# Optimization experiments

Hardware: AMD Instinct MI355X
Metric: run time of the kernel (lower is better)

The kernel has to match this reference:

```python
import jax, jax.numpy as jnp
import numpy as np

T_TOTAL = 90  # t_total init arg (static decode length)


def _gru_cell(x, h, w_ih, w_hh, b_ih, b_hh):
    # PyTorch nn.GRUCell math
    gi = x @ w_ih.T + b_ih
    gh = h @ w_hh.T + b_hh
    i_r, i_z, i_n = jnp.split(gi, 3, axis=-1)
    h_r, h_z, h_n = jnp.split(gh, 3, axis=-1)
    r = jax.nn.sigmoid(i_r + h_r)
    z = jax.nn.sigmoid(i_z + h_z)
    n = jnp.tanh(i_n + r * h_n)
    return (1.0 - z) * n + z * h


def setup_inputs() -> dict:
    key = jax.random.key(0)
    T, B, NX, H, NZ = 90, 2048, 144, 128, 128
    M1, M2 = 300, 200
    ks = jax.random.split(key, 24)
    def p(k, shape):
        return jax.random.normal(k, shape, dtype=jnp.float32) * 0.05
    return {
        "x": jax.random.normal(ks[0], (T, B, NX), dtype=jnp.float32),
        # encoder GRUCell (nx -> H)
        "w_ih_e": p(ks[1], (3 * H, NX)), "w_hh_e": p(ks[2], (3 * H, H)),
        "b_ih_e": p(ks[3], (3 * H,)),   "b_hh_e": p(ks[4], (3 * H,)),
        # encoder MLP (tanh) H->300->200
        "W1e": p(ks[5], (M1, H)),  "b1e": p(ks[6], (M1,)),
        "W2e": p(ks[7], (M2, M1)), "b2e": p(ks[8], (M2,)),
        # latent heads 200->NZ
        "Wmu": p(ks[9], (NZ, M2)),  "bmu": p(ks[10], (NZ,)),
        "Wlv": p(ks[11], (NZ, M2)), "blv": p(ks[12], (NZ,)),
        # decoder GRUCell (nx+nz -> H)
        "w_ih_d": p(ks[13], (3 * H, NX + NZ)), "w_hh_d": p(ks[14], (3 * H, H)),
        "b_ih_d": p(ks[15], (3 * H,)),          "b_hh_d": p(ks[16], (3 * H,)),
        # decoder MLP (tanh) H->300->200 and output 200->nx
        "W1d": p(ks[17], (M1, H)),  "b1d": p(ks[18], (M1,)),
        "W2d": p(ks[19], (M2, M1)), "b2d": p(ks[20], (M2,)),
        "Wo": p(ks[21], (NX, M2)),  "bo": p(ks[22], (NX,)),
    }


def reference(x, w_ih_e, w_hh_e, b_ih_e, b_hh_e, W1e, b1e, W2e, b2e,
              Wmu, bmu, Wlv, blv, w_ih_d, w_hh_d, b_ih_d, b_hh_d,
              W1d, b1d, W2d, b2d, Wo, bo):
    B = x.shape[1]
    H = w_hh_e.shape[1]
    h0 = jnp.zeros((B, H), dtype=x.dtype)

    # ---- encode: GRU over time, take last hidden ----
    def enc_step(h, xt):
        return _gru_cell(xt, h, w_ih_e, w_hh_e, b_ih_e, b_hh_e), None
    h_x, _ = jax.lax.scan(enc_step, h0, x)  # (B, H)
    he = jnp.tanh(h_x @ W1e.T + b1e)
    he = jnp.tanh(he @ W2e.T + b2e)
    mu = he @ Wmu.T + bmu
    logvar = he @ Wlv.T + blv
    z = mu  # eval mode: z = mu (no reparameterization noise)

    def dec_step(carry, _):
        hd, xp = carry
        rnn_in = jnp.concatenate([xp, z], axis=1)  # (B, NX+NZ)
        hd = _gru_cell(rnn_in, hd, w_ih_d, w_hh_d, b_ih_d, b_hh_d)
        m = jnp.tanh(hd @ W1d.T + b1d)
        m = jnp.tanh(m @ W2d.T + b2d)
        xi = m @ Wo.T + bo
        return (hd, xi), xi

    _, x_rec = jax.lax.scan(dec_step, (h0, x[0]), None, length=T_TOTAL)
    return x_rec, mu, logvar
```

## Files before the change

### kernel.cpp

```cpp
#include <hip/hip_runtime.h>
#include <cstddef>

#define T_STEPS 90
#define BT      2048
#define NXV     144
#define HV      128
#define NZV     128
#define M1V     300
#define M2V     200
#define NB      16
#define NTH     512

typedef __attribute__((ext_vector_type(8))) _Float16 half8v;
typedef __attribute__((ext_vector_type(4))) float f32x4;

constexpr int MTa[12]   = {24,24,19,13, 8, 8,24,24,24,19,13, 9};
constexpr int MREAL[12] = {384,384,300,200,128,128,384,384,384,300,200,144};
constexpr int KREAL[12] = {144,128,128,300,200,200,144,128,128,128,300,200};
constexpr int RSW[12]   = {144,128,128,300,200,200,272,272,128,128,300,200};
constexpr int COW[12]   = {  0,  0,  0,  0,  0,  0,  0,144,  0,  0,  0,  0};
constexpr int P13[13]   = {0,120,240,335,465,521,577,697,817,937,1032,1162,1225};
constexpr int NFRAG = 1225;

__device__ __forceinline__ float fsig(float v)  { return 1.0f / (1.0f + __expf(-v)); }
__device__ __forceinline__ float ftanh(float v) { return 1.0f - 2.0f / (__expf(2.0f * v) + 1.0f); }

__global__ void __launch_bounds__(64)
prep_frags(const float* __restrict__ w_ih_e, const float* __restrict__ w_hh_e,
           const float* __restrict__ W1e,    const float* __restrict__ W2e,
           const float* __restrict__ Wmu,    const float* __restrict__ Wlv,
           const float* __restrict__ w_ih_d, const float* __restrict__ w_hh_d,
           const float* __restrict__ W1d,    const float* __restrict__ W2d,
           const float* __restrict__ Wo,
           const float* __restrict__ b_ih_e, const float* __restrict__ b_hh_e,
           const float* __restrict__ b1e,    const float* __restrict__ b2e,
           const float* __restrict__ bmu,    const float* __restrict__ blv,
           const float* __restrict__ b_ih_d, const float* __restrict__ b_hh_d,
           const float* __restrict__ b1d,    const float* __restrict__ b2d,
           const float* __restrict__ bo,
           _Float16* __restrict__ ws)
{
    int f = blockIdx.x;
    int g = 0;
    while (g < 11 && f >= P13[g + 1]) ++g;
    int fl = f - P13[g];
    int MT = MTa[g];
    int kt = fl / MT, mt = fl - kt * MT;

    const float* W; const float* bias;
    switch (g) {
        case 0:  W = w_ih_e; bias = b_ih_e; break;
        case 1:  W = w_hh_e; bias = b_hh_e; break;
        case 2:  W = W1e;    bias = b1e;    break;
        case 3:  W = W2e;    bias = b2e;    break;
        case 4:  W = Wmu;    bias = bmu;    break;
        case 5:  W = Wlv;    bias = blv;    break;
        case 6:  W = w_ih_d; bias = nullptr; break;
        case 7:  W = w_ih_d; bias = b_ih_d; break;
        case 8:  W = w_hh_d; bias = b_hh_d; break;
        case 9:  W = W1d;    bias = b1d;    break;
        case 10: W = W2d;    bias = b2d;    break;
        default: W = Wo;     bias = bo;     break;
    }
    int l = threadIdx.x;
    int m  = mt * 16 + (l & 15);
    int kb = kt * 32 + (l >> 4) * 8;
    _Float16* dst = ws + (size_t)f * 512 + (size_t)l * 8;
    #pragma unroll
    for (int j = 0; j < 8; ++j) {
        int k = kb + j;
        float val = 0.0f;
        if (m < MREAL[g]) {
            if (k < KREAL[g]) val = W[(size_t)m * RSW[g] + COW[g] + k];
            else if (k == KREAL[g] && bias) val = bias[m];
        }
        dst[j] = (_Float16)val;
    }
}

template<int RS>
__device__ __forceinline__ void gate_gemm_reg(const half8v (&gw)[15],
                                              const _Float16* __restrict__ Bt,
                                              int l, f32x4 (&acc)[3])
{
    const int bo_ = (l & 15) * RS + ((l >> 4) << 3);
    #pragma unroll
    for (int kt = 0; kt < 5; ++kt) {
        half8v bf = *(const half8v*)(Bt + bo_ + kt * 32);
        #pragma unroll
        for (int j = 0; j < 3; ++j)
            acc[j] = __builtin_amdgcn_mfma_f32_16x16x32_f16(gw[kt * 3 + j], bf, acc[j], 0, 0, 0);
    }
}

template<int MT, int KT, int NT, int RS>
__device__ __forceinline__ void mlp_stream(const half8v* __restrict__ A,
                                           const _Float16* __restrict__ Bt,
                                           int w, int l, f32x4 (&acc)[NT])
{
    half8v af[NT * KT];
    #pragma unroll
    for (int i = 0; i < NT; ++i) {
        int mt = w + 8 * i;
        if (mt < MT) {
            #pragma unroll
            for (int kt = 0; kt < KT; ++kt)
                af[i * KT + kt] = A[(size_t)(kt * MT + mt) * 64 + l];
        }
    }
    const int bo_ = (l & 15) * RS + ((l >> 4) << 3);
    #pragma unroll
    for (int kt = 0; kt < KT; ++kt) {
        half8v bf = *(const half8v*)(Bt + bo_ + kt * 32);
        #pragma unroll
        for (int i = 0; i < NT; ++i) {
            int mt = w + 8 * i;
            if (mt < MT)
                acc[i] = __builtin_amdgcn_mfma_f32_16x16x32_f16(af[i * KT + kt], bf, acc[i], 0, 0, 0);
        }
    }
}

template<int MT, int KT, int NT, int RS>
__device__ __forceinline__ void mlp_lds(const _Float16* __restrict__ Alds,
                                        const _Float16* __restrict__ Bt,
                                        int w, int l, f32x4 (&acc)[NT])
{
    const int bo_ = (l & 15) * RS + ((l >> 4) << 3);
    #pragma unroll
    for (int kt = 0; kt < KT; ++kt) {
        half8v bf = *(const half8v*)(Bt + bo_ + kt * 32);
        #pragma unroll
        for (int i = 0; i < NT; ++i) {
            int mt = w + 8 * i;
            if (mt < MT) {
                half8v af = *(const half8v*)(Alds + ((size_t)(kt * MT + mt) * 64 + l) * 8);
                acc[i] = __builtin_amdgcn_mfma_f32_16x16x32_f16(af, bf, acc[i], 0, 0, 0);
            }
        }
    }
}

template<int MT, int NT, int RS>
__device__ __forceinline__ void write_tanhN(const f32x4 (&acc)[NT], int Mreal,
                                            _Float16* __restrict__ T, int w, int l)
{
    int b = l & 15, q4 = (l >> 4) << 2;
    #pragma unroll
    for (int i = 0; i < NT; ++i) {
        int mt = w + 8 * i;
        if (mt < MT) {
            #pragma unroll
            for (int r = 0; r < 4; ++r) {
                int m = mt * 16 + q4 + r;
                if (m < Mreal) T[b * RS + m] = (_Float16)ftanh(acc[i][r]);
            }
        }
    }
}

__global__ void __launch_bounds__(NTH, 2)
vae_mfma(const float* __restrict__ x, const half8v* __restrict__ wsv,
         float* __restrict__ out)
{
    __shared__ __align__(16) _Float16 xT [NB * 168];
    __shared__ __align__(16) _Float16 hT [NB * 168];
    __shared__ __align__(16) _Float16 m1T[NB * 328];
    __shared__ __align__(16) _Float16 m2T[NB * 232];
    __shared__ __align__(16) _Float16 g10L[130 * 512];

    const int tid = threadIdx.x;
    const int w = tid >> 6, l = tid & 63;
    const int bbase = blockIdx.x * NB;
    const size_t XREC_SZ = (size_t)T_STEPS * BT * NXV;
    const size_t MU_OFF = XREC_SZ;
    const size_t LV_OFF = XREC_SZ + (size_t)BT * NZV;
    const f32x4 z4 = {0.f, 0.f, 0.f, 0.f};

#define AHI(g) (wsv + (size_t)P13[g] * 64)

    auto load_x = [&](int t, float xr[5]) {
        #pragma unroll
        for (int u = 0; u < 5; ++u) {
            int i = u * NTH + tid;
            if (i < NB * NXV)
                xr[u] = __builtin_nontemporal_load(
                    &x[(size_t)t * (BT * NXV) + (size_t)(bbase + i / NXV) * NXV + (i % NXV)]);
        }
    };
    auto store_x = [&](const float xr[5]) {
        #pragma unroll
        for (int u = 0; u < 5; ++u) {
            int i = u * NTH + tid;
            if (i < NB * NXV) {
                int b2 = i / NXV, k = i - b2 * NXV;
                xT[b2 * 168 + k] = (_Float16)xr[u];
            }
        }
    };

    half8v gih[15], ghh[15];
    auto load_gates = [&](const half8v* Gih, const half8v* Ghh) {
        #pragma unroll
        for (int kt = 0; kt < 5; ++kt) {
            #pragma unroll
            for (int j = 0; j < 3; ++j) {
                gih[kt * 3 + j] = Gih[(size_t)(kt * 24 + w + 8 * j) * 64 + l];
                ghh[kt * 3 + j] = Ghh[(size_t)(kt * 24 + w + 8 * j) * 64 + l];
            }
        }
    };

    float hreg[4] = {0.f, 0.f, 0.f, 0.f};
    auto gru_combine = [&](const f32x4 (&ai)[3], const f32x4 (&ah)[3]) {
        #pragma unroll
        for (int r = 0; r < 4; ++r) {
            float rr = fsig(ai[0][r] + ah[0][r]);
            float zz = fsig(ai[1][r] + ah[1][r]);
            float nn = ftanh(ai[2][r] + rr * ah[2][r]);
            hreg[r] = (1.f - zz) * nn + zz * hreg[r];
        }
    };
    auto write_h = [&]() {
        int jb = 16 * w + ((l >> 4) << 2), b = l & 15;
        #pragma unroll
        for (int r = 0; r < 4; ++r) hT[b * 168 + jb + r] = (_Float16)hreg[r];
    };

    for (int i = tid; i < NB * 168; i += NTH) { xT[i] = (_Float16)0.f; hT[i] = (_Float16)0.f; }
    for (int i = tid; i < NB * 328; i += NTH) m1T[i] = (_Float16)0.f;
    for (int i = tid; i < NB * 232; i += NTH) m2T[i] = (_Float16)0.f;
    for (int i = tid; i < 130 * 64; i += NTH)
        *(half8v*)(g10L + (size_t)i * 8) = AHI(10)[i];
    load_gates(AHI(0), AHI(1));
    float xrA[5] = {0, 0, 0, 0, 0}, xrB[5] = {0, 0, 0, 0, 0};
    load_x(0, xrA);
    __syncthreads();
    if (tid < NB) {
        xT [tid * 168 + 144] = (_Float16)1.f;
        hT [tid * 168 + 128] = (_Float16)1.f;
        m1T[tid * 328 + 300] = (_Float16)1.f;
        m2T[tid * 232 + 200] = (_Float16)1.f;
    }
    store_x(xrA);
    load_x(1, xrA);
    __syncthreads();

    for (int t = 0; t < T_STEPS; t += 2) {
        {
            if (t + 2 < T_STEPS) load_x(t + 2, xrB);
            f32x4 ai[3] = {z4, z4, z4}, ah[3] = {z4, z4, z4};
            gate_gemm_reg<168>(gih, xT, l, ai);
            gate_gemm_reg<168>(ghh, hT, l, ah);
            gru_combine(ai, ah);
            __syncthreads();
            write_h();
            if (t + 1 < T_STEPS) store_x(xrA);
            __syncthreads();
        }
        {
            if (t + 3 < T_STEPS) load_x(t + 3, xrA);
            f32x4 ai[3] = {z4, z4, z4}, ah[3] = {z4, z4, z4};
            gate_gemm_reg<168>(gih, xT, l, ai);
            gate_gemm_reg<168>(ghh, hT, l, ah);
            gru_combine(ai, ah);
            __syncthreads();
            write_h();
            if (t + 2 < T_STEPS) store_x(xrB);
            __syncthreads();
        }
    }

    {
        f32x4 a1[3] = {z4, z4, z4};
        mlp_stream<19, 5, 3, 168>(AHI(2), hT, w, l, a1);
        write_tanhN<19, 3, 328>(a1, M1V, m1T, w, l);
        __syncthreads();
        f32x4 a2[2] = {z4, z4};
        mlp_stream<13, 10, 2, 328>(AHI(3), m1T, w, l, a2);
        write_tanhN<13, 2, 232>(a2, M2V, m2T, w, l);
        __syncthreads();
        f32x4 am[1] = {z4}, av[1] = {z4};
        mlp_stream<8, 7, 1, 232>(AHI(4), m2T, w, l, am);
        mlp_stream<8, 7, 1, 232>(AHI(5), m2T, w, l, av);
        __syncthreads();
        int b = l & 15, q4 = (l >> 4) << 2;
        int m = w * 16 + q4;
        __builtin_nontemporal_store(am[0], (f32x4*)&out[MU_OFF + (size_t)(bbase + b) * NZV + m]);
        __builtin_nontemporal_store(av[0], (f32x4*)&out[LV_OFF + (size_t)(bbase + b) * NZV + m]);
        #pragma unroll
        for (int r = 0; r < 4; ++r)
            m1T[b * 328 + m + r] = (_Float16)am[0][r];
    }

    f32x4 gzr[3] = {z4, z4, z4};
    {
        for (int i = tid; i < NB * HV; i += NTH) {
            int b2 = i >> 7, j = i & 127;
            hT[b2 * 168 + j] = (_Float16)0.f;
        }
        if (tid < NB) m1T[tid * 328 + 128] = (_Float16)1.f;
        float xr0[5] = {0, 0, 0, 0, 0};
        load_x(0, xr0);
        store_x(xr0);
        __syncthreads();
        mlp_stream<24, 5, 3, 328>(AHI(7), m1T, w, l, gzr);
        load_gates(AHI(6), AHI(8));
        #pragma unroll
        for (int r = 0; r < 4; ++r) hreg[r] = 0.f;
    }
    __syncthreads();

    f32x4 aop[2] = {z4, z4};
    for (int t = 0; t < T_STEPS; ++t) {
        if (t > 0 && w < 9) {
            int b = l & 15, q4 = (l >> 4) << 2;
            #pragma unroll
            for (int i2 = 0; i2 < 2; ++i2) {
                int mt = w + 8 * i2;
                if (mt < 9)
                    __builtin_nontemporal_store(aop[i2],
                        (f32x4*)&out[(size_t)(t - 1) * (BT * NXV) + (size_t)(bbase + b) * NXV + mt * 16 + q4]);
            }
        }
        f32x4 ai[3], ah[3];
        #pragma unroll
        for (int i = 0; i < 3; ++i) { ai[i] = gzr[i]; ah[i] = z4; }
        gate_gemm_reg<168>(gih, xT, l, ai);
        gate_gemm_reg<168>(ghh, hT, l, ah);
        gru_combine(ai, ah);
        __syncthreads();
        write_h();
        __syncthreads();
        f32x4 a1[3] = {z4, z4, z4};
        mlp_stream<19, 5, 3, 168>(AHI(9), hT, w, l, a1);
        write_tanhN<19, 3, 328>(a1, M1V, m1T, w, l);
        __syncthreads();
        f32x4 a2[2] = {z4, z4};
        mlp_lds<13, 10, 2, 328>(g10L, m1T, w, l, a2);
        write_tanhN<13, 2, 232>(a2, M2V, m2T, w, l);
        __syncthreads();
        f32x4 ao[2] = {z4, z4};
        mlp_stream<9, 7, 2, 232>(AHI(11), m2T, w, l, ao);
        {
            int b = l & 15, q4 = (l >> 4) << 2;
            #pragma unroll
            for (int i2 = 0; i2 < 2; ++i2) {
                int mt = w + 8 * i2;
                if (mt < 9) {
                    int m = mt * 16 + q4;
                    #pragma unroll
                    for (int r = 0; r < 4; ++r)
                        xT[b * 168 + m + r] = (_Float16)ao[i2][r];
                    aop[i2] = ao[i2];
                }
            }
        }
        __syncthreads();
    }
    if (w < 9) {
        int b = l & 15, q4 = (l >> 4) << 2;
        #pragma unroll
        for (int i2 = 0; i2 < 2; ++i2) {
            int mt = w + 8 * i2;
            if (mt < 9)
                __builtin_nontemporal_store(aop[i2],
                    (f32x4*)&out[(size_t)(T_STEPS - 1) * (BT * NXV) + (size_t)(bbase + b) * NXV + mt * 16 + q4]);
        }
    }
#undef AHI
}

extern "C" void kernel_launch(void* const* d_in, const int* in_sizes, int n_in,
                              void* d_out, int out_size, void* d_ws, size_t ws_size,
                              hipStream_t stream) {
    (void)in_sizes; (void)n_in; (void)out_size; (void)ws_size;
    const float* p[23];
    for (int i = 0; i < 23; ++i) p[i] = (const float*)d_in[i];
    _Float16* ws = (_Float16*)d_ws;

    prep_frags<<<dim3(NFRAG), dim3(64), 0, stream>>>(
        p[1], p[2], p[5], p[7], p[9], p[11], p[13], p[14], p[17], p[19], p[21],
        p[3], p[4], p[6], p[8], p[10], p[12], p[15], p[16], p[18], p[20], p[22],
        ws);

    vae_mfma<<<dim3(BT / NB), dim3(NTH), 0, stream>>>(
        p[0], (const half8v*)ws, (float*)d_out);
}
```

Baseline: 866.2 us.

## Double-buffer decoder hidden state and prefetch output-layer weights into registers

Makes the decoder hidden-state LDS tile double-buffered (ping-pong on step parity), which removes one block barrier per decode step before writing h. It also shrinks the LDS copy of the W2d weights by one K-tile, streaming that last tile from global into registers early, and prefetches all Wo fragments into registers before the W2d GEMM so the output GEMM runs from registers. These changes hide global-load latency and drop a sync, in exchange for extra LDS for the second h buffer and higher register pressure that could lower occupancy at launch bounds (512, 2).

```diff
diff --git a/kernel.cpp b/kernel.cpp
--- a/kernel.cpp
+++ b/kernel.cpp
@@ -164,10 +164,10 @@
          float* __restrict__ out)
 {
     __shared__ __align__(16) _Float16 xT [NB * 168];
-    __shared__ __align__(16) _Float16 hT [NB * 168];
+    __shared__ __align__(16) _Float16 hT [2][NB * 168];
     __shared__ __align__(16) _Float16 m1T[NB * 328];
     __shared__ __align__(16) _Float16 m2T[NB * 232];
-    __shared__ __align__(16) _Float16 g10L[130 * 512];
+    __shared__ __align__(16) _Float16 g10L[117 * 512];
 
     const int tid = threadIdx.x;
     const int w = tid >> 6, l = tid & 63;
@@ -221,16 +221,16 @@
             hreg[r] = (1.f - zz) * nn + zz * hreg[r];
         }
     };
-    auto write_h = [&]() {
+    auto write_h = [&](int p) {
         int jb = 16 * w + ((l >> 4) << 2), b = l & 15;
         #pragma unroll
-        for (int r = 0; r < 4; ++r) hT[b * 168 + jb + r] = (_Float16)hreg[r];
+        for (int r = 0; r < 4; ++r) hT[p][b * 168 + jb + r] = (_Float16)hreg[r];
     };
 
-    for (int i = tid; i < NB * 168; i += NTH) { xT[i] = (_Float16)0.f; hT[i] = (_Float16)0.f; }
+    for (int i = tid; i < NB * 168; i += NTH) { xT[i] = (_Float16)0.f; hT[0][i] = (_Float16)0.f; hT[1][i] = (_Float16)0.f; }
     for (int i = tid; i < NB * 328; i += NTH) m1T[i] = (_Float16)0.f;
     for (int i = tid; i < NB * 232; i += NTH) m2T[i] = (_Float16)0.f;
-    for (int i = tid; i < 130 * 64; i += NTH)
+    for (int i = tid; i < 117 * 64; i += NTH)
         *(half8v*)(g10L + (size_t)i * 8) = AHI(10)[i];
     load_gates(AHI(0), AHI(1));
     float xrA[5] = {0, 0, 0, 0, 0}, xrB[5] = {0, 0, 0, 0, 0};
@@ -238,7 +238,8 @@
     __syncthreads();
     if (tid < NB) {
         xT [tid * 168 + 144] = (_Float16)1.f;
-        hT [tid * 168 + 128] = (_Float16)1.f;
+        hT[0][tid * 168 + 128] = (_Float16)1.f;
+        hT[1][tid * 168 + 128] = (_Float16)1.f;
         m1T[tid * 328 + 300] = (_Float16)1.f;
         m2T[tid * 232 + 200] = (_Float16)1.f;
     }
@@ -251,10 +252,10 @@
             if (t + 2 < T_STEPS) load_x(t + 2, xrB);
             f32x4 ai[3] = {z4, z4, z4}, ah[3] = {z4, z4, z4};
             gate_gemm_reg<168>(gih, xT, l, ai);
-            gate_gemm_reg<168>(ghh, hT, l, ah);
+            gate_gemm_reg<168>(ghh, hT[0], l, ah);
             gru_combine(ai, ah);
             __syncthreads();
-            write_h();
+            write_h(0);
             if (t + 1 < T_STEPS) store_x(xrA);
             __syncthreads();
         }
@@ -262,10 +263,10 @@
             if (t + 3 < T_STEPS) load_x(t + 3, xrA);
             f32x4 ai[3] = {z4, z4, z4}, ah[3] = {z4, z4, z4};
             gate_gemm_reg<168>(gih, xT, l, ai);
-            gate_gemm_reg<168>(ghh, hT, l, ah);
+            gate_gemm_reg<168>(ghh, hT[0], l, ah);
             gru_combine(ai, ah);
             __syncthreads();
-            write_h();
+            write_h(0);
             if (t + 2 < T_STEPS) store_x(xrB);
             __syncthreads();
         }
@@ -273,7 +274,7 @@
 
     {
         f32x4 a1[3] = {z4, z4, z4};
-        mlp_stream<19, 5, 3, 168>(AHI(2), hT, w, l, a1);
+        mlp_stream<19, 5, 3, 168>(AHI(2), hT[0], w, l, a1);
         write_tanhN<19, 3, 328>(a1, M1V, m1T, w, l);
         __syncthreads();
         f32x4 a2[2] = {z4, z4};
@@ -297,7 +298,7 @@
     {
         for (int i = tid; i < NB * HV; i += NTH) {
             int b2 = i >> 7, j = i & 127;
-            hT[b2 * 168 + j] = (_Float16)0.f;
+            hT[0][b2 * 168 + j] = (_Float16)0.f;
         }
         if (tid < NB) m1T[tid * 328 + 128] = (_Float16)1.f;
         float xr0[5] = {0, 0, 0, 0, 0};
@@ -313,6 +314,7 @@
 
     f32x4 aop[2] = {z4, z4};
     for (int t = 0; t < T_STEPS; ++t) {
+        const int q = t & 1;
         if (t > 0 && w < 9) {
             int b = l & 15, q4 = (l >> 4) << 2;
             #pragma unroll
@@ -327,21 +329,51 @@
         #pragma unroll
         for (int i = 0; i < 3; ++i) { ai[i] = gzr[i]; ah[i] = z4; }
         gate_gemm_reg<168>(gih, xT, l, ai);
-        gate_gemm_reg<168>(ghh, hT, l, ah);
+        gate_gemm_reg<168>(ghh, hT[q], l, ah);
         gru_combine(ai, ah);
-        __syncthreads();
-        write_h();
-        __syncthreads();
+        write_h(q ^ 1);
+        __syncthreads();
+        half8v w2f9[2];
+        #pragma unroll
+        for (int i = 0; i < 2; ++i)
+            if (w + 8 * i < 13)
+                w2f9[i] = AHI(10)[(size_t)(9 * 13 + w + 8 * i) * 64 + l];
         f32x4 a1[3] = {z4, z4, z4};
-        mlp_stream<19, 5, 3, 168>(AHI(9), hT, w, l, a1);
+        mlp_stream<19, 5, 3, 168>(AHI(9), hT[q ^ 1], w, l, a1);
         write_tanhN<19, 3, 328>(a1, M1V, m1T, w, l);
         __syncthreads();
+        half8v wo_af[14];
+        #pragma unroll
+        for (int kt = 0; kt < 7; ++kt) {
+            #pragma unroll
+            for (int i = 0; i < 2; ++i)
+                if (w + 8 * i < 9)
+                    wo_af[kt * 2 + i] = AHI(11)[(size_t)(kt * 9 + w + 8 * i) * 64 + l];
+        }
         f32x4 a2[2] = {z4, z4};
-        mlp_lds<13, 10, 2, 328>(g10L, m1T, w, l, a2);
+        mlp_lds<13, 9, 2, 328>(g10L, m1T, w, l, a2);
+        {
+            const int bo2 = (l & 15) * 328 + ((l >> 4) << 3);
+            half8v bf = *(const half8v*)(m1T + bo2 + 9 * 32);
+            #pragma unroll
+            for (int i = 0; i < 2; ++i)
+                if (w + 8 * i < 13)
+                    a2[i] = __builtin_amdgcn_mfma_f32_16x16x32_f16(w2f9[i], bf, a2[i], 0, 0, 0);
+        }
         write_tanhN<13, 2, 232>(a2, M2V, m2T, w, l);
         __syncthreads();
         f32x4 ao[2] = {z4, z4};
-        mlp_stream<9, 7, 2, 232>(AHI(11), m2T, w, l, ao);
+        {
+            const int bo_ = (l & 15) * 232 + ((l >> 4) << 3);
+            #pragma unroll
+            for (int kt = 0; kt < 7; ++kt) {
+                half8v bf = *(const half8v*)(m2T + bo_ + kt * 32);
+                #pragma unroll
+                for (int i = 0; i < 2; ++i)
+                    if (w + 8 * i < 9)
+                        ao[i] = __builtin_amdgcn_mfma_f32_16x16x32_f16(wo_af[kt * 2 + i], bf, ao[i], 0, 0, 0);
+            }
+        }
         {
             int b = l & 15, q4 = (l >> 4) << 2;
             #pragma unroll
```

New measurement: 1.091 ms. 26.0% more time.

## Fold decoder output projection into next-step GRU input weights

Applied to the files above, without the earlier changes.

Precomputes combined weights (w_ih_d[:, :NX] @ Wo, plus the bias term) in the prep kernel so that each decoder step's input gate consumes the MLP hidden m2 directly instead of the reconstructed output. This removes the per-step write of the output into the xT LDS buffer and one block barrier, and decouples the output GEMM from the next step's gate computation. In exchange, the input gate GEMM now streams K=200 weights from memory rather than using register-resident K=144 fragments, and fp16 rounding differs.

```diff
diff --git a/kernel.cpp b/kernel.cpp
--- a/kernel.cpp
+++ b/kernel.cpp
@@ -21,6 +21,7 @@
 constexpr int COW[12]   = {  0,  0,  0,  0,  0,  0,  0,144,  0,  0,  0,  0};
 constexpr int P13[13]   = {0,120,240,335,465,521,577,697,817,937,1032,1162,1225};
 constexpr int NFRAG = 1225;
+constexpr int NFRAG2 = NFRAG + 24 * 7;
 
 __device__ __forceinline__ float fsig(float v)  { return 1.0f / (1.0f + __expf(-v)); }
 __device__ __forceinline__ float ftanh(float v) { return 1.0f - 2.0f / (__expf(2.0f * v) + 1.0f); }
@@ -41,6 +42,30 @@
            _Float16* __restrict__ ws)
 {
     int f = blockIdx.x;
+    int l = threadIdx.x;
+    if (f >= NFRAG) {
+        int fl = f - NFRAG;
+        int kt = fl / 24, mt = fl - kt * 24;
+        int m  = mt * 16 + (l & 15);
+        int kb = kt * 32 + (l >> 4) * 8;
+        _Float16* dst = ws + (size_t)f * 512 + (size_t)l * 8;
+        #pragma unroll
+        for (int j = 0; j < 8; ++j) {
+            int k = kb + j;
+            float val = 0.0f;
+            if (m < 384) {
+                if (k < M2V) {
+                    for (int j2 = 0; j2 < NXV; ++j2)
+                        val += w_ih_d[(size_t)m * 272 + j2] * Wo[(size_t)j2 * M2V + k];
+                } else if (k == M2V) {
+                    for (int j2 = 0; j2 < NXV; ++j2)
+                        val += w_ih_d[(size_t)m * 272 + j2] * bo[j2];
+                }
+            }
+            dst[j] = (_Float16)val;
+        }
+        return;
+    }
     int g = 0;
     while (g < 11 && f >= P13[g + 1]) ++g;
     int fl = f - P13[g];
@@ -62,7 +87,6 @@
         case 10: W = W2d;    bias = b2d;    break;
         default: W = Wo;     bias = bo;     break;
     }
-    int l = threadIdx.x;
     int m  = mt * 16 + (l & 15);
     int kb = kt * 32 + (l >> 4) * 8;
     _Float16* dst = ws + (size_t)f * 512 + (size_t)l * 8;
@@ -178,6 +202,7 @@
     const f32x4 z4 = {0.f, 0.f, 0.f, 0.f};
 
 #define AHI(g) (wsv + (size_t)P13[g] * 64)
+#define ACMB   (wsv + (size_t)NFRAG * 64)
 
     auto load_x = [&](int t, float xr[5]) {
         #pragma unroll
@@ -209,6 +234,13 @@
                 ghh[kt * 3 + j] = Ghh[(size_t)(kt * 24 + w + 8 * j) * 64 + l];
             }
         }
+    };
+    auto load_ghh = [&](const half8v* Ghh) {
+        #pragma unroll
+        for (int kt = 0; kt < 5; ++kt)
+            #pragma unroll
+            for (int j = 0; j < 3; ++j)
+                ghh[kt * 3 + j] = Ghh[(size_t)(kt * 24 + w + 8 * j) * 64 + l];
     };
 
     float hreg[4] = {0.f, 0.f, 0.f, 0.f};
@@ -305,28 +337,49 @@
         store_x(xr0);
         __syncthreads();
         mlp_stream<24, 5, 3, 328>(AHI(7), m1T, w, l, gzr);
-        load_gates(AHI(6), AHI(8));
+        load_ghh(AHI(8));
         #pragma unroll
         for (int r = 0; r < 4; ++r) hreg[r] = 0.f;
     }
     __syncthreads();
 
-    f32x4 aop[2] = {z4, z4};
-    for (int t = 0; t < T_STEPS; ++t) {
-        if (t > 0 && w < 9) {
+    {
+        f32x4 ai[3], ah[3];
+        #pragma unroll
+        for (int i = 0; i < 3; ++i) { ai[i] = gzr[i]; ah[i] = z4; }
+        mlp_stream<24, 5, 3, 168>(AHI(6), xT, w, l, ai);
+        gate_gemm_reg<168>(ghh, hT, l, ah);
+        gru_combine(ai, ah);
+        __syncthreads();
+        write_h();
+        __syncthreads();
+        f32x4 a1[3] = {z4, z4, z4};
+        mlp_stream<19, 5, 3, 168>(AHI(9), hT, w, l, a1);
+        write_tanhN<19, 3, 328>(a1, M1V, m1T, w, l);
+        __syncthreads();
+        f32x4 a2[2] = {z4, z4};
+        mlp_lds<13, 10, 2, 328>(g10L, m1T, w, l, a2);
+        write_tanhN<13, 2, 232>(a2, M2V, m2T, w, l);
+        __syncthreads();
+    }
+
+    for (int t = 1; t < T_STEPS; ++t) {
+        {
+            f32x4 ao[2] = {z4, z4};
+            mlp_stream<9, 7, 2, 232>(AHI(11), m2T, w, l, ao);
             int b = l & 15, q4 = (l >> 4) << 2;
             #pragma unroll
             for (int i2 = 0; i2 < 2; ++i2) {
                 int mt = w + 8 * i2;
                 if (mt < 9)
-                    __builtin_nontemporal_store(aop[i2],
+                    __builtin_nontemporal_store(ao[i2],
                         (f32x4*)&out[(size_t)(t - 1) * (BT * NXV) + (size_t)(bbase + b) * NXV + mt * 16 + q4]);
             }
         }
         f32x4 ai[3], ah[3];
         #pragma unroll
         for (int i = 0; i < 3; ++i) { ai[i] = gzr[i]; ah[i] = z4; }
-        gate_gemm_reg<168>(gih, xT, l, ai);
+        mlp_stream<24, 7, 3, 232>(ACMB, m2T, w, l, ai);
         gate_gemm_reg<168>(ghh, hT, l, ah);
         gru_combine(ai, ah);
         __syncthreads();
@@ -340,35 +393,21 @@
         mlp_lds<13, 10, 2, 328>(g10L, m1T, w, l, a2);
         write_tanhN<13, 2, 232>(a2, M2V, m2T, w, l);
         __syncthreads();
+    }
+    {
         f32x4 ao[2] = {z4, z4};
         mlp_stream<9, 7, 2, 232>(AHI(11), m2T, w, l, ao);
-        {
-            int b = l & 15, q4 = (l >> 4) << 2;
-            #pragma unroll
-            for (int i2 = 0; i2 < 2; ++i2) {
-                int mt = w + 8 * i2;
-                if (mt < 9) {
-                    int m = mt * 16 + q4;
-                    #pragma unroll
-                    for (int r = 0; r < 4; ++r)
-                        xT[b * 168 + m + r] = (_Float16)ao[i2][r];
-                    aop[i2] = ao[i2];
-                }
-            }
-        }
-        __syncthreads();
-    }
-    if (w < 9) {
         int b = l & 15, q4 = (l >> 4) << 2;
         #pragma unroll
         for (int i2 = 0; i2 < 2; ++i2) {
             int mt = w + 8 * i2;
             if (mt < 9)
-                __builtin_nontemporal_store(aop[i2],
+                __builtin_nontemporal_store(ao[i2],
                     (f32x4*)&out[(size_t)(T_STEPS - 1) * (BT * NXV) + (size_t)(bbase + b) * NXV + mt * 16 + q4]);
         }
     }
 #undef AHI
+#undef ACMB
 }
 
 extern "C" void kernel_launch(void* const* d_in, const int* in_sizes, int n_in,
@@ -379,7 +418,7 @@
     for (int i = 0; i < 23; ++i) p[i] = (const float*)d_in[i];
     _Float16* ws = (_Float16*)d_ws;
 
-    prep_frags<<<dim3(NFRAG), dim3(64), 0, stream>>>(
+    prep_frags<<<dim3(NFRAG2), dim3(64), 0, stream>>>(
         p[1], p[2], p[5], p[7], p[9], p[11], p[13], p[14], p[17], p[19], p[21],
         p[3], p[4], p[6], p[8], p[10], p[12], p[15], p[16], p[18], p[20], p[22],
         ws);
```

New measurement: 932.6 us. 1.08x slower.
